# Kernel optimization log

Hardware: AMD Instinct MI355X
Metric: run time of the kernel (lower is better)

Reference implementation:

```python
import jax, jax.numpy as jnp
import numpy as np

IMG = 512
B = 4
NA = 3          # anchors per location
NC = 3          # classes
K = 512         # pre-NMS top-k per image per level (<= smallest level anchor count 768)
STRIDES = [4, 8, 16, 32]
MIN_S = [0.01, 0.02, 0.03, 0.04]
MAX_S = [0.06, 0.08, 0.10, 0.12]
W_SC = [0.8, 0.9, 1.0, 1.1]
H_SC = [1.0, 1.2, 1.4, 1.6]
CONF_T = 0.15
NMS_T = 0.5
STD = 0.2       # box_delta_stds (means are 0)


def make_anchors(stride):
    H = IMG // stride
    c = (np.arange(H) + 0.5) * stride
    cy, cx = np.meshgrid(c, c, indexing='ij')           # [H, W]
    sizes = stride * 4.0 * (2.0 ** (np.arange(NA) / 3.0))  # [A]
    cx = np.broadcast_to(cx, (NA, H, H))
    cy = np.broadcast_to(cy, (NA, H, H))
    s = sizes[:, None, None]
    # A-major, then H, W -- matches permute(0,1,3,4,2).reshape flattening
    anc = np.stack([cx - s / 2, cy - s / 2, cx + s / 2, cy + s / 2], -1).reshape(-1, 4)
    return jnp.asarray(anc, jnp.float32)


def setup_inputs() -> dict:
    key = jax.random.key(0)
    ks = jax.random.split(key, 8)
    inp = {}
    for l, s in enumerate(STRIDES):
        H = IMG // s
        inp[f'cls{l}'] = jax.random.normal(ks[2 * l], (B, NA, NC, H, H), jnp.float32)
        inp[f'box{l}'] = jax.random.normal(ks[2 * l + 1], (B, NA, 4, H, H), jnp.float32)
        inp[f'anc{l}'] = make_anchors(s)
    inp['image_size'] = IMG
    return inp


def decode_level(cls, box, anc, lvl, image_size):
    Bc, A, C, H, W = cls.shape
    scores = jax.nn.sigmoid(jnp.transpose(cls, (0, 1, 3, 4, 2)).reshape(Bc, -1, C))  # [B,N,C]
    d = jnp.transpose(box, (0, 1, 3, 4, 2)).reshape(Bc, -1, 4)                        # [B,N,4]
    img = jnp.asarray(image_size, jnp.float32)
    aw = (anc[:, 2] - anc[:, 0]) / img
    ah = (anc[:, 3] - anc[:, 1]) / img
    acx = (anc[:, 0] + anc[:, 2]) * 0.5 / img
    acy = (anc[:, 1] + anc[:, 3]) * 0.5 / img
    fs = 1.0 / STRIDES[lvl]
    dx = jnp.clip(d[..., 0] * STD, -1.0, 1.0) * fs * aw
    dy = jnp.clip(d[..., 1] * STD, -1.0, 1.0) * fs * ah
    cx = jnp.clip(acx + dx, 0.0, 1.0)
    cy = jnp.clip(acy + dy, 0.0, 1.0)
    dw = jnp.clip(d[..., 2] * STD, -2.0, 2.0)
    dh = jnp.clip(d[..., 3] * STD, -2.0, 2.0)
    pw = jnp.clip(aw * W_SC[lvl] * jnp.exp(dw * (0.2 + 0.1 * lvl)), MIN_S[lvl] * 0.8, MAX_S[lvl] * 0.9)
    ph = jnp.clip(ah * H_SC[lvl] * jnp.exp(dh * (0.4 + 0.2 * lvl)), MIN_S[lvl] * 0.8, MAX_S[lvl] * 1.2)
    boxes = jnp.stack([
        jnp.clip(cx - 0.5 * pw, 0.0, 1.0),
        jnp.clip(cy - 0.5 * ph, 0.0, 1.0),
        jnp.clip(cx + 0.5 * pw, 0.0, 1.0),
        jnp.clip(cy + 0.5 * ph, 0.0, 1.0)], -1)                                       # [B,N,4]
    ms = scores.max(-1)
    mc = scores.argmax(-1)
    w = boxes[..., 2] - boxes[..., 0]
    h = boxes[..., 3] - boxes[..., 1]
    valid = (ms > CONF_T) & (w > MIN_S[lvl] * 0.5) & (h > MIN_S[lvl] * 0.5) \
            & (w < MAX_S[lvl] * 2.0) & (h < MAX_S[lvl] * 2.0)
    # pre-NMS top-k on (masked) scores
    sort_key = jnp.where(valid, ms, -1.0)
    _, idx = jax.lax.top_k(sort_key, K)                                               # [B,K]
    boxes_k = jnp.take_along_axis(boxes, idx[..., None], 1)
    scores_k = jnp.take_along_axis(ms, idx, 1)
    labels_k = jnp.take_along_axis(mc, idx, 1)
    valid_k = jnp.take_along_axis(valid, idx, 1)
    return boxes_k, scores_k, labels_k, valid_k


def pairwise_iou(b):
    area = (b[:, 2] - b[:, 0]) * (b[:, 3] - b[:, 1])
    lt = jnp.maximum(b[:, None, :2], b[None, :, :2])
    rb = jnp.minimum(b[:, None, 2:], b[None, :, 2:])
    wh = jnp.clip(rb - lt, 0.0)
    inter = wh[..., 0] * wh[..., 1]
    return inter / (area[:, None] + area[None, :] - inter + 1e-9)


def nms_keep(boxes, valid):
    # boxes sorted by descending score; sequential greedy NMS
    iou = pairwise_iou(boxes)                 # [K,K]
    rank = jnp.arange(K)
    def body(i, keep):
        overlap = jnp.max(jnp.where((rank < i) & keep, iou[i], 0.0))
        return keep.at[i].set(valid[i] & (overlap <= NMS_T))
    return jax.lax.fori_loop(0, K, body, jnp.zeros((K,), bool))


def reference(cls0, box0, anc0, cls1, box1, anc1, cls2, box2, anc2, cls3, box3, anc3, image_size):
    levels = [(cls0, box0, anc0), (cls1, box1, anc1), (cls2, box2, anc2), (cls3, box3, anc3)]
    outs = [decode_level(c, b, a, l, image_size) for l, (c, b, a) in enumerate(levels)]
    boxes = jnp.stack([o[0] for o in outs], 1)    # [B, L, K, 4]
    scores = jnp.stack([o[1] for o in outs], 1)   # [B, L, K]
    labels = jnp.stack([o[2] for o in outs], 1)   # [B, L, K]
    valid = jnp.stack([o[3] for o in outs], 1)    # [B, L, K]
    keep = jax.vmap(jax.vmap(nms_keep))(boxes, valid)
    boxes = jnp.where(keep[..., None], boxes, 0.0)
    scores = jnp.where(keep, scores, 0.0)
    labels = jnp.where(keep, labels + 1, 0)       # torch code returns labels + 1
    return boxes, scores, labels, keep
```

## Files before the change

### kernel.cpp

```cpp
#include <hip/hip_runtime.h>
#include <math.h>

#define K_TOP 512
#define CAND_CAP 3072

struct LvlC {
  int H, lgH, HH, lgHH;
  float fs, wsc, hsc, wex, hex, pwlo, pwhi, phlo, phhi, minwh, maxwh;
};

__device__ const LvlC LVL[4] = {
  {128, 7, 16384, 14, 0.25f,    0.8f, 1.0f, 0.2f, 0.4f, 0.008f, 0.054f, 0.008f, 0.072f, 0.005f, 0.12f},
  { 64, 6,  4096, 12, 0.125f,   0.9f, 1.2f, 0.3f, 0.6f, 0.016f, 0.072f, 0.016f, 0.096f, 0.01f,  0.16f},
  { 32, 5,  1024, 10, 0.0625f,  1.0f, 1.4f, 0.4f, 0.8f, 0.024f, 0.09f,  0.024f, 0.12f,  0.015f, 0.2f },
  { 16, 4,   256,  8, 0.03125f, 1.1f, 1.6f, 0.5f, 1.0f, 0.032f, 0.108f, 0.032f, 0.144f, 0.02f,  0.24f},
};

__device__ const float TSEL[4] = {0.91f, 0.85f, 0.65f, -2.0f};

__device__ __forceinline__ void decode_box(const LvlC& L, const float* __restrict__ boxp,
                                           const float* __restrict__ ancp,
                                           int b, int idx, float rimg,
                                           float& x0, float& y0, float& x1, float& y1)
{
#pragma clang fp contract(off)
  int a   = idx >> L.lgHH;
  int rem = idx & (L.HH - 1);
  const float* bp = boxp + (size_t)((b * 3 + a) * 4) * L.HH + rem;
  float d0 = bp[0], d1 = bp[L.HH], d2 = bp[2 * L.HH], d3 = bp[3 * L.HH];
  float4 av = reinterpret_cast<const float4*>(ancp)[idx];
  float a0 = av.x, a1 = av.y, a2 = av.z, a3 = av.w;
  float aw  = (a2 - a0) * rimg;
  float ah  = (a3 - a1) * rimg;
  float acx = (a0 + a2) * 0.5f * rimg;
  float acy = (a1 + a3) * 0.5f * rimg;
  float dx = fminf(fmaxf(d0 * 0.2f, -1.f), 1.f) * L.fs * aw;
  float dy = fminf(fmaxf(d1 * 0.2f, -1.f), 1.f) * L.fs * ah;
  float cx = fminf(fmaxf(acx + dx, 0.f), 1.f);
  float cy = fminf(fmaxf(acy + dy, 0.f), 1.f);
  float dw = fminf(fmaxf(d2 * 0.2f, -2.f), 2.f);
  float dh = fminf(fmaxf(d3 * 0.2f, -2.f), 2.f);
  float pw = fminf(fmaxf(aw * L.wsc * expf(dw * L.wex), L.pwlo), L.pwhi);
  float ph = fminf(fmaxf(ah * L.hsc * expf(dh * L.hex), L.phlo), L.phhi);
  x0 = fminf(fmaxf(cx - 0.5f * pw, 0.f), 1.f);
  y0 = fminf(fmaxf(cy - 0.5f * ph, 0.f), 1.f);
  x1 = fminf(fmaxf(cx + 0.5f * pw, 0.f), 1.f);
  y1 = fminf(fmaxf(cy + 0.5f * ph, 0.f), 1.f);
}

__device__ __forceinline__ void seg_map(int blk, int& b, int& l, int& base, int& iblk)
{
  b = blk / 255;
  int rb = blk - b * 255;
  if (rb < 192)      { l = 0; iblk = rb;       base = 0;     }
  else if (rb < 240) { l = 1; iblk = rb - 192; base = 49152; }
  else if (rb < 252) { l = 2; iblk = rb - 240; base = 61440; }
  else               { l = 3; iblk = rb - 252; base = 64512; }
}

__global__ __launch_bounds__(256) void dc_kernel(
    const float* __restrict__ cls0, const float* __restrict__ box0, const float* __restrict__ anc0,
    const float* __restrict__ cls1, const float* __restrict__ box1, const float* __restrict__ anc1,
    const float* __restrict__ cls2, const float* __restrict__ box2, const float* __restrict__ anc2,
    const float* __restrict__ cls3, const float* __restrict__ box3, const float* __restrict__ anc3,
    const int* __restrict__ imgp, unsigned long long* __restrict__ keys,
    unsigned long long* __restrict__ cand, unsigned* __restrict__ unitCnt)
{
  __shared__ unsigned wcnt[4];
  int unit = (int)blockIdx.x;
  int tid = (int)threadIdx.x;
  int wid = tid >> 6, lane = tid & 63;
  int b, l, base, iblk;
  seg_map(unit, b, l, base, iblk);
  int i = iblk * 256 + tid;

  const float *cls, *boxp, *ancp;
  switch (l) {
    case 0:  cls = cls0; boxp = box0; ancp = anc0; break;
    case 1:  cls = cls1; boxp = box1; ancp = anc1; break;
    case 2:  cls = cls2; boxp = box2; ancp = anc2; break;
    default: cls = cls3; boxp = box3; ancp = anc3; break;
  }
  LvlC L = LVL[l];
  float rimg = 1.0f / (float)(*imgp);

  int a   = i >> L.lgHH;
  int rem = i & (L.HH - 1);
  const float* cp = cls + (size_t)((b * 3 + a) * 3) * L.HH + rem;
  float c0 = cp[0], c1 = cp[L.HH], c2 = cp[2 * L.HH];
  float m = c0; int mc = 0;
  if (c1 > m) { m = c1; mc = 1; }
  if (c2 > m) { m = c2; mc = 2; }
  float ms = 1.f / (1.f + expf(-m));

  float x0, y0, x1, y1;
  decode_box(L, boxp, ancp, b, i, rimg, x0, y0, x1, y1);
  float w = x1 - x0, h = y1 - y0;
  bool valid = (ms > 0.15f) && (w > L.minwh) && (h > L.minwh) && (w < L.maxwh) && (h < L.maxwh);

  float sk = valid ? ms : -1.0f;
  unsigned u = __float_as_uint(sk);
  unsigned ascu  = (u & 0x80000000u) ? ~u : (u | 0x80000000u);
  unsigned descu = ~ascu;
  unsigned long long key = ((unsigned long long)descu << 32)
                         | ((unsigned long long)(unsigned)i << 16)
                         | ((unsigned)mc << 8) | (valid ? 1u : 0u);
  keys[(size_t)b * 65280 + base + i] = key;

  bool take = (sk >= TSEL[l]);
  unsigned long long bm = __ballot(take);
  if (lane == 0) wcnt[wid] = (unsigned)__popcll(bm);
  __syncthreads();
  if (take) {
    unsigned off = 0;
    for (int w2 = 0; w2 < wid; ++w2) off += wcnt[w2];
    off += (unsigned)__popcll(bm & ((1ull << lane) - 1ull));
    cand[(size_t)unit * 256 + off] = key;
  }
  if (tid == 0) unitCnt[unit] = wcnt[0] + wcnt[1] + wcnt[2] + wcnt[3];
}

__global__ __launch_bounds__(512) void sel_kernel(
    const unsigned long long* __restrict__ keys,
    const unsigned long long* __restrict__ cand, const unsigned* __restrict__ unitCnt,
    const float* __restrict__ box0, const float* __restrict__ anc0,
    const float* __restrict__ box1, const float* __restrict__ anc1,
    const float* __restrict__ box2, const float* __restrict__ anc2,
    const float* __restrict__ box3, const float* __restrict__ anc3,
    const int* __restrict__ imgp,
    float* __restrict__ boxesWS, float* __restrict__ scoresWS,
    int* __restrict__ labelsWS, unsigned* __restrict__ validWS)
{
  __shared__ unsigned long long scand[CAND_CAP];
  __shared__ unsigned long long skey[K_TOP];
  __shared__ unsigned long long skey2[K_TOP];
  __shared__ unsigned hist[8][256];
  __shared__ unsigned upref[256];
  __shared__ unsigned ucnt_s[256];
  __shared__ unsigned waveSum[8];
  __shared__ unsigned long long shPrefix;
  __shared__ unsigned shBelow, shCnt, shTotal;

  int seg = (int)blockIdx.x;
  int b = seg >> 2, l = seg & 3;
  int tid = (int)threadIdx.x;
  const int nt = 512;
  int wid = tid >> 6, lane = tid & 63;

  const int nArr[4]    = {49152, 12288, 3072, 768};
  const int baseArr[4] = {0, 49152, 61440, 64512};
  const int nuArr[4]   = {192, 48, 12, 3};
  const int fuArr[4]   = {0, 192, 240, 252};
  int N = nArr[l];
  int nu = nuArr[l];
  int firstU = b * 255 + fuArr[l];
  const unsigned long long* kp = keys + (size_t)b * 65280 + baseArr[l];

  if (tid == 0) { shPrefix = 0ull; shBelow = 0u; shCnt = 0u; }

  unsigned c = (tid < nu) ? unitCnt[firstU + tid] : 0u;
  if (tid < 256) ucnt_s[tid] = c;
  unsigned incl = c;
  for (int off = 1; off < 64; off <<= 1) {
    unsigned n = __shfl_up(incl, off);
    if (lane >= off) incl += n;
  }
  if (lane == 63) waveSum[wid] = incl;
  __syncthreads();
  if (tid < 256) {
    unsigned add = 0;
    for (int w2 = 0; w2 < wid; ++w2) add += waveSum[w2];
    if (tid < nu) upref[tid] = incl - c + add;
  }
  if (tid == 0) shTotal = waveSum[0] + waveSum[1] + waveSum[2] + waveSum[3];
  __syncthreads();

  unsigned total = shTotal;
  bool useCand = (total >= K_TOP && total <= CAND_CAP);
  int M = useCand ? (int)total : N;

  if (useCand) {
    for (int f = tid; f < (int)total; f += nt) {
      int lo = 0, hi = nu - 1;
      while (lo < hi) {
        int mid = (lo + hi + 1) >> 1;
        if ((int)upref[mid] <= f) lo = mid; else hi = mid - 1;
      }
      scand[f] = cand[(size_t)(firstU + lo) * 256 + (unsigned)(f - (int)upref[lo])];
    }
  }
  __syncthreads();

  for (int r = 0; r < 6; ++r) {
    int shift = 56 - 8 * r;
    for (int v = tid; v < 8 * 256; v += nt) ((unsigned*)hist)[v] = 0u;
    __syncthreads();
    unsigned long long pref = shPrefix;
    unsigned below = shBelow;
    unsigned long long hiMask = (r == 0) ? 0ull : (~0ull << (64 - 8 * r));
    for (int t = tid; t < M; t += nt) {
      unsigned long long k = useCand ? scand[t] : kp[t];
      if ((k & hiMask) == (pref & hiMask))
        atomicAdd(&hist[wid][(unsigned)((k >> shift) & 0xFF)], 1u);
    }
    __syncthreads();
    unsigned s = 0, incl2 = 0;
    if (tid < 256) {
#pragma unroll
      for (int w2 = 0; w2 < 8; ++w2) s += hist[w2][tid];
      incl2 = s;
    }
    for (int off = 1; off < 64; off <<= 1) {
      unsigned n = __shfl_up(incl2, off);
      if (lane >= off) incl2 += n;
    }
    if (lane == 63) waveSum[wid] = incl2;
    __syncthreads();
    if (tid < 256) {
      unsigned add = 0;
      for (int w2 = 0; w2 < wid; ++w2) add += waveSum[w2];
      unsigned inclT = incl2 + add;
      unsigned exclT = inclT - s;
      if (below + exclT < K_TOP && below + inclT >= K_TOP) {
        shBelow = below + exclT;
        shPrefix = pref | ((unsigned long long)(unsigned)tid << shift);
      }
    }
    __syncthreads();
  }
  unsigned long long kth = shPrefix | 0xFFFFull;

  for (int t = tid; t < M; t += nt) {
    unsigned long long k = useCand ? scand[t] : kp[t];
    bool take = (k <= kth);
    unsigned long long bm = __ballot(take);
    unsigned bp = 0;
    if (lane == 0 && bm) bp = atomicAdd(&shCnt, (unsigned)__popcll(bm));
    bp = __shfl(bp, 0);
    if (take) skey[bp + (unsigned)__popcll(bm & ((1ull << lane) - 1ull))] = k;
  }
  __syncthreads();

  {
    unsigned long long mykey = skey[tid];
    int rank = 0;
#pragma unroll 8
    for (int j = 0; j < K_TOP; ++j) rank += (skey[j] < mykey) ? 1 : 0;
    skey2[rank] = mykey;
  }
  __syncthreads();

  const float *boxp, *ancp;
  switch (l) {
    case 0:  boxp = box0; ancp = anc0; break;
    case 1:  boxp = box1; ancp = anc1; break;
    case 2:  boxp = box2; ancp = anc2; break;
    default: boxp = box3; ancp = anc3; break;
  }
  LvlC L = LVL[l];
  float rimg = 1.0f / (float)(*imgp);
  {
    unsigned long long key = skey2[tid];
    int idx = (int)((key >> 16) & 0xFFFFull);
    unsigned descu = (unsigned)(key >> 32);
    unsigned ascu  = ~descu;
    unsigned u = (ascu & 0x80000000u) ? (ascu & 0x7FFFFFFFu) : ~ascu;
    float x0, y0, x1, y1;
    decode_box(L, boxp, ancp, b, idx, rimg, x0, y0, x1, y1);
    int o = seg * K_TOP + tid;
    float4 bb; bb.x = x0; bb.y = y0; bb.z = x1; bb.w = y1;
    reinterpret_cast<float4*>(boxesWS)[o] = bb;
    scoresWS[o] = __uint_as_float(u);
    labelsWS[o] = (int)((key >> 8) & 0xFFull);
    validWS[o]  = (unsigned)(key & 1ull);
  }
}

__global__ __launch_bounds__(256) void mask_kernel(
    const float* __restrict__ boxesWS, unsigned long long* __restrict__ masks)
{
#pragma clang fp contract(off)
  int blk = (int)blockIdx.x;
  int seg = blk >> 5;
  int wid = (int)threadIdx.x >> 6;
  int lane = (int)threadIdx.x & 63;
  int waveInSeg = (blk & 31) * 4 + wid;
  const float4* bb = reinterpret_cast<const float4*>(boxesWS) + seg * K_TOP;
  unsigned long long* mseg = masks + (size_t)seg * K_TOP * 8;

  float4 bj[8]; float aj[8];
#pragma unroll
  for (int c = 0; c < 8; ++c) {
    bj[c] = bb[c * 64 + lane];
    aj[c] = (bj[c].z - bj[c].x) * (bj[c].w - bj[c].y);
  }
#pragma unroll
  for (int rr = 0; rr < 4; ++rr) {
    int r = waveInSeg * 4 + rr;
    float4 br = bb[r];
    float ar_ = (br.z - br.x) * (br.w - br.y);
#pragma unroll
    for (int c = 0; c < 8; ++c) {
      float ltx = fmaxf(br.x, bj[c].x), lty = fmaxf(br.y, bj[c].y);
      float rbx = fminf(br.z, bj[c].z), rby = fminf(br.w, bj[c].w);
      float ww = fmaxf(rbx - ltx, 0.f), hh = fmaxf(rby - lty, 0.f);
      float inter = ww * hh;
      float iou = inter / (ar_ + aj[c] - inter + 1e-9f);
      unsigned long long bal = __ballot(iou > 0.5f);
      if (lane == 0) mseg[c * K_TOP + r] = bal;
    }
  }
}

__global__ __launch_bounds__(512) void scan_kernel(
    const unsigned long long* __restrict__ masks,
    const float* __restrict__ boxesWS, const float* __restrict__ scoresWS,
    const int* __restrict__ labelsWS, const unsigned* __restrict__ validWS,
    float* __restrict__ out)
{
  __shared__ unsigned long long sMaskT[8 * K_TOP];
  __shared__ unsigned long long keepWords[8];
  __shared__ unsigned sChanged;

  int seg = (int)blockIdx.x;
  int tid = (int)threadIdx.x;
  int wid = tid >> 6, lane = tid & 63;
  const unsigned long long* mp = masks + (size_t)seg * K_TOP * 8;
#pragma unroll
  for (int w = 0; w < 8; ++w) sMaskT[w * K_TOP + tid] = mp[w * K_TOP + tid];
  bool valid = validWS[seg * K_TOP + tid] != 0u;

  unsigned long long myWord = __ballot(valid);
  if (lane == 0) keepWords[wid] = myWord;
  __syncthreads();

  for (int it = 0; it < 513; ++it) {
    unsigned long long sup = 0ull;
    for (int w = 0; w < wid; ++w)
      sup |= sMaskT[w * K_TOP + tid] & keepWords[w];
    sup |= sMaskT[wid * K_TOP + tid] & keepWords[wid] & ((1ull << lane) - 1ull);
    bool nk = valid && (sup == 0ull);
    unsigned long long nw = __ballot(nk);
    __syncthreads();
    if (tid == 0) sChanged = 0u;
    __syncthreads();
    if (lane == 0) {
      if (nw != keepWords[wid]) sChanged = 1u;
      keepWords[wid] = nw;
    }
    __syncthreads();
    if (sChanged == 0u) break;
  }

  int o = seg * K_TOP + tid;
  bool keep = (keepWords[wid] >> lane) & 1ull;
  float4 bx = reinterpret_cast<const float4*>(boxesWS)[o];
  float4 ob;
  ob.x = keep ? bx.x : 0.f;
  ob.y = keep ? bx.y : 0.f;
  ob.z = keep ? bx.z : 0.f;
  ob.w = keep ? bx.w : 0.f;
  reinterpret_cast<float4*>(out)[o] = ob;
  out[32768 + o] = keep ? scoresWS[o] : 0.f;
  out[40960 + o] = keep ? (float)(labelsWS[o] + 1) : 0.f;
  out[49152 + o] = keep ? 1.f : 0.f;
}

extern "C" void kernel_launch(void* const* d_in, const int* in_sizes, int n_in,
                              void* d_out, int out_size, void* d_ws, size_t ws_size,
                              hipStream_t stream)
{
  const float* cls0 = (const float*)d_in[0];
  const float* box0 = (const float*)d_in[1];
  const float* anc0 = (const float*)d_in[2];
  const float* cls1 = (const float*)d_in[3];
  const float* box1 = (const float*)d_in[4];
  const float* anc1 = (const float*)d_in[5];
  const float* cls2 = (const float*)d_in[6];
  const float* box2 = (const float*)d_in[7];
  const float* anc2 = (const float*)d_in[8];
  const float* cls3 = (const float*)d_in[9];
  const float* box3 = (const float*)d_in[10];
  const float* anc3 = (const float*)d_in[11];
  const int*   imgp = (const int*)d_in[12];

  char* ws = (char*)d_ws;
  unsigned long long* keys    = (unsigned long long*)(ws + 0);
  unsigned long long* cand    = (unsigned long long*)(ws + 2088960);
  unsigned*           unitCnt = (unsigned*)(ws + 4177920);
  float*              boxesWS = (float*)(ws + 4182016);
  float*              scoresWS= (float*)(ws + 4313088);
  int*                labelsWS= (int*)(ws + 4345856);
  unsigned*           validWS = (unsigned*)(ws + 4378624);
  unsigned long long* masks   = (unsigned long long*)(ws + 4411392);
  float* out = (float*)d_out;

  dc_kernel<<<1020, 256, 0, stream>>>(cls0, box0, anc0, cls1, box1, anc1,
                                      cls2, box2, anc2, cls3, box3, anc3,
                                      imgp, keys, cand, unitCnt);
  sel_kernel<<<16, 512, 0, stream>>>(keys, cand, unitCnt,
                                     box0, anc0, box1, anc1, box2, anc2, box3, anc3,
                                     imgp, boxesWS, scoresWS, labelsWS, validWS);
  mask_kernel<<<512, 256, 0, stream>>>(boxesWS, masks);
  scan_kernel<<<16, 512, 0, stream>>>(masks, boxesWS, scoresWS, labelsWS, validWS, out);
}
```

Baseline: 118.0 us.

## Fuse top-k selection and IoU mask kernels with redundant per-block selection

Merges the selection kernel and the IoU mask kernel into one launch of 512 blocks. Each of the 32 blocks per segment redoes the radix top-k selection and box decode, keeps the sorted boxes in shared memory through a union with the candidate buffer, then computes its own 16 rows of the suppression mask. This removes one kernel launch and the global round trip of the boxes, and spreads the selection over many more blocks. The cost is 32x redundant selection work and heavier global reads of keys and candidates.

```diff
diff --git a/kernel.cpp b/kernel.cpp
--- a/kernel.cpp
+++ b/kernel.cpp
@@ -120,7 +120,7 @@
   if (tid == 0) unitCnt[unit] = wcnt[0] + wcnt[1] + wcnt[2] + wcnt[3];
 }
 
-__global__ __launch_bounds__(512) void sel_kernel(
+__global__ __launch_bounds__(512) void selmask_kernel(
     const unsigned long long* __restrict__ keys,
     const unsigned long long* __restrict__ cand, const unsigned* __restrict__ unitCnt,
     const float* __restrict__ box0, const float* __restrict__ anc0,
@@ -129,9 +129,14 @@
     const float* __restrict__ box3, const float* __restrict__ anc3,
     const int* __restrict__ imgp,
     float* __restrict__ boxesWS, float* __restrict__ scoresWS,
-    int* __restrict__ labelsWS, unsigned* __restrict__ validWS)
-{
-  __shared__ unsigned long long scand[CAND_CAP];
+    int* __restrict__ labelsWS, unsigned* __restrict__ validWS,
+    unsigned long long* __restrict__ masks)
+{
+  union SelU {
+    unsigned long long scand[CAND_CAP];
+    float4 sBox[K_TOP];
+  };
+  __shared__ SelU su;
   __shared__ unsigned long long skey[K_TOP];
   __shared__ unsigned long long skey2[K_TOP];
   __shared__ unsigned hist[8][256];
@@ -141,7 +146,9 @@
   __shared__ unsigned long long shPrefix;
   __shared__ unsigned shBelow, shCnt, shTotal;
 
-  int seg = (int)blockIdx.x;
+  int blk = (int)blockIdx.x;
+  int seg = blk >> 5;
+  int sub = blk & 31;
   int b = seg >> 2, l = seg & 3;
   int tid = (int)threadIdx.x;
   const int nt = 512;
@@ -186,7 +193,7 @@
         int mid = (lo + hi + 1) >> 1;
         if ((int)upref[mid] <= f) lo = mid; else hi = mid - 1;
       }
-      scand[f] = cand[(size_t)(firstU + lo) * 256 + (unsigned)(f - (int)upref[lo])];
+      su.scand[f] = cand[(size_t)(firstU + lo) * 256 + (unsigned)(f - (int)upref[lo])];
     }
   }
   __syncthreads();
@@ -199,7 +206,7 @@
     unsigned below = shBelow;
     unsigned long long hiMask = (r == 0) ? 0ull : (~0ull << (64 - 8 * r));
     for (int t = tid; t < M; t += nt) {
-      unsigned long long k = useCand ? scand[t] : kp[t];
+      unsigned long long k = useCand ? su.scand[t] : kp[t];
       if ((k & hiMask) == (pref & hiMask))
         atomicAdd(&hist[wid][(unsigned)((k >> shift) & 0xFF)], 1u);
     }
@@ -231,7 +238,7 @@
   unsigned long long kth = shPrefix | 0xFFFFull;
 
   for (int t = tid; t < M; t += nt) {
-    unsigned long long k = useCand ? scand[t] : kp[t];
+    unsigned long long k = useCand ? su.scand[t] : kp[t];
     bool take = (k <= kth);
     unsigned long long bm = __ballot(take);
     unsigned bp = 0;
@@ -250,6 +257,9 @@
   }
   __syncthreads();
 
+  unsigned long long key = skey2[tid];
+  __syncthreads();
+
   const float *boxp, *ancp;
   switch (l) {
     case 0:  boxp = box0; ancp = anc0; break;
@@ -260,54 +270,48 @@
   LvlC L = LVL[l];
   float rimg = 1.0f / (float)(*imgp);
   {
-    unsigned long long key = skey2[tid];
     int idx = (int)((key >> 16) & 0xFFFFull);
     unsigned descu = (unsigned)(key >> 32);
     unsigned ascu  = ~descu;
     unsigned u = (ascu & 0x80000000u) ? (ascu & 0x7FFFFFFFu) : ~ascu;
     float x0, y0, x1, y1;
     decode_box(L, boxp, ancp, b, idx, rimg, x0, y0, x1, y1);
-    int o = seg * K_TOP + tid;
     float4 bb; bb.x = x0; bb.y = y0; bb.z = x1; bb.w = y1;
-    reinterpret_cast<float4*>(boxesWS)[o] = bb;
-    scoresWS[o] = __uint_as_float(u);
-    labelsWS[o] = (int)((key >> 8) & 0xFFull);
-    validWS[o]  = (unsigned)(key & 1ull);
-  }
-}
-
-__global__ __launch_bounds__(256) void mask_kernel(
-    const float* __restrict__ boxesWS, unsigned long long* __restrict__ masks)
-{
+    su.sBox[tid] = bb;
+    if (sub == 0) {
+      int o = seg * K_TOP + tid;
+      reinterpret_cast<float4*>(boxesWS)[o] = bb;
+      scoresWS[o] = __uint_as_float(u);
+      labelsWS[o] = (int)((key >> 8) & 0xFFull);
+      validWS[o]  = (unsigned)(key & 1ull);
+    }
+  }
+  __syncthreads();
+
+  {
 #pragma clang fp contract(off)
-  int blk = (int)blockIdx.x;
-  int seg = blk >> 5;
-  int wid = (int)threadIdx.x >> 6;
-  int lane = (int)threadIdx.x & 63;
-  int waveInSeg = (blk & 31) * 4 + wid;
-  const float4* bb = reinterpret_cast<const float4*>(boxesWS) + seg * K_TOP;
-  unsigned long long* mseg = masks + (size_t)seg * K_TOP * 8;
-
-  float4 bj[8]; float aj[8];
+    unsigned long long* mseg = masks + (size_t)seg * K_TOP * 8;
+    float4 bj[8]; float aj[8];
 #pragma unroll
-  for (int c = 0; c < 8; ++c) {
-    bj[c] = bb[c * 64 + lane];
-    aj[c] = (bj[c].z - bj[c].x) * (bj[c].w - bj[c].y);
-  }
+    for (int cc = 0; cc < 8; ++cc) {
+      bj[cc] = su.sBox[cc * 64 + lane];
+      aj[cc] = (bj[cc].z - bj[cc].x) * (bj[cc].w - bj[cc].y);
+    }
 #pragma unroll
-  for (int rr = 0; rr < 4; ++rr) {
-    int r = waveInSeg * 4 + rr;
-    float4 br = bb[r];
-    float ar_ = (br.z - br.x) * (br.w - br.y);
+    for (int rr = 0; rr < 2; ++rr) {
+      int r = sub * 16 + wid * 2 + rr;
+      float4 br = su.sBox[r];
+      float ar_ = (br.z - br.x) * (br.w - br.y);
 #pragma unroll
-    for (int c = 0; c < 8; ++c) {
-      float ltx = fmaxf(br.x, bj[c].x), lty = fmaxf(br.y, bj[c].y);
-      float rbx = fminf(br.z, bj[c].z), rby = fminf(br.w, bj[c].w);
-      float ww = fmaxf(rbx - ltx, 0.f), hh = fmaxf(rby - lty, 0.f);
-      float inter = ww * hh;
-      float iou = inter / (ar_ + aj[c] - inter + 1e-9f);
-      unsigned long long bal = __ballot(iou > 0.5f);
-      if (lane == 0) mseg[c * K_TOP + r] = bal;
+      for (int cc = 0; cc < 8; ++cc) {
+        float ltx = fmaxf(br.x, bj[cc].x), lty = fmaxf(br.y, bj[cc].y);
+        float rbx = fminf(br.z, bj[cc].z), rby = fminf(br.w, bj[cc].w);
+        float ww = fmaxf(rbx - ltx, 0.f), hh = fmaxf(rby - lty, 0.f);
+        float inter = ww * hh;
+        float iou = inter / (ar_ + aj[cc] - inter + 1e-9f);
+        unsigned long long bal = __ballot(iou > 0.5f);
+        if (lane == 0) mseg[cc * K_TOP + r] = bal;
+      }
     }
   }
 }
@@ -398,9 +402,8 @@
   dc_kernel<<<1020, 256, 0, stream>>>(cls0, box0, anc0, cls1, box1, anc1,
                                       cls2, box2, anc2, cls3, box3, anc3,
                                       imgp, keys, cand, unitCnt);
-  sel_kernel<<<16, 512, 0, stream>>>(keys, cand, unitCnt,
-                                     box0, anc0, box1, anc1, box2, anc2, box3, anc3,
-                                     imgp, boxesWS, scoresWS, labelsWS, validWS);
-  mask_kernel<<<512, 256, 0, stream>>>(boxesWS, masks);
+  selmask_kernel<<<512, 512, 0, stream>>>(keys, cand, unitCnt,
+                                          box0, anc0, box1, anc1, box2, anc2, box3, anc3,
+                                          imgp, boxesWS, scoresWS, labelsWS, validWS, masks);
   scan_kernel<<<16, 512, 0, stream>>>(masks, boxesWS, scoresWS, labelsWS, validWS, out);
 }
```

After: 120.2 us. No clear change (+1.8%).
